# Optimization experiments

Measured on AMD Instinct MI355X. Metric: run time of the kernel, lower is better.

## Reference

```python
import jax, jax.numpy as jnp
import numpy as np

EPS_BN = 1e-5      # torch BatchNorm2d default eps
EPSILON = 1e-12    # signed-sqrt eps from the module
K = 3              # hardcoded k in forward


def _knn_idx(f, k):
    # f: [B, C, N] -> idx [B, N, k] of nearest neighbors (largest -dist^2)
    xx = jnp.sum(f * f, axis=1)                      # [B, N]
    inner = jnp.einsum('bcn,bcm->bnm', f, f)         # [B, N, N]
    pd = -xx[:, :, None] + 2.0 * inner - xx[:, None, :]
    return jax.lax.top_k(pd, k)[1]                   # [B, N, k]


def _graph_feature(f, k):
    # f: [B, C, N] -> [B, N, k, 2C] = concat(neighbor - center, center)
    idx = _knn_idx(f, k)
    ft = jnp.transpose(f, (0, 2, 1))                 # [B, N, C]
    neigh = jax.vmap(lambda x, i: x[i])(ft, idx)     # [B, N, k, C]
    center = jnp.broadcast_to(ft[:, :, None, :], neigh.shape)
    return jnp.concatenate([neigh - center, center], axis=-1)


def _edgeconv(f, W, gamma, beta, mean, var, k):
    # f: [B, C, N]; W: [O, 2C] (1x1 conv, no bias); eval-mode BN; LeakyReLU(0.2); max over k
    g = _graph_feature(f, k)                         # [B, N, k, 2C]
    y = jnp.einsum('bnkc,oc->bonk', g, W)            # [B, O, N, k]
    scale = (gamma / jnp.sqrt(var + EPS_BN))[None, :, None, None]
    y = (y - mean[None, :, None, None]) * scale + beta[None, :, None, None]
    y = jnp.where(y >= 0, y, 0.2 * y)                # LeakyReLU(0.2)
    return jnp.max(y, axis=-1)                       # [B, O, N]


def setup_inputs() -> dict:
    key = jax.random.key(0)
    ks = jax.random.split(key, 12)
    B, C, H, W, M = 64, 768, 26, 26, 32
    inp = {
        'features': jax.random.normal(ks[0], (B, C, H, W), jnp.float32),
        'attentions': jax.random.uniform(ks[1], (B, M, H, W), jnp.float32),
        'W1': jax.random.normal(ks[2], (C, 2 * C), jnp.float32) * 0.02,
        'gamma1': jax.random.uniform(ks[3], (C,), jnp.float32, 0.5, 1.5),
        'beta1': jax.random.normal(ks[4], (C,), jnp.float32) * 0.1,
        'mean1': jax.random.normal(ks[5], (C,), jnp.float32) * 0.1,
        'var1': jax.random.uniform(ks[6], (C,), jnp.float32, 0.5, 1.5),
        'W2': jax.random.normal(ks[7], (C, 2 * C), jnp.float32) * 0.02,
        'gamma2': jax.random.uniform(ks[8], (C,), jnp.float32, 0.5, 1.5),
        'beta2': jax.random.normal(ks[9], (C,), jnp.float32) * 0.1,
        'mean2': jax.random.normal(ks[10], (C,), jnp.float32) * 0.1,
        'var2': jax.random.uniform(ks[11], (C,), jnp.float32, 0.5, 1.5),
    }
    return inp


def reference(features, attentions, W1, gamma1, beta1, mean1, var1,
              W2, gamma2, beta2, mean2, var2):
    B = features.shape[0]
    # AdaptiveMaxPool2d(1) of features * attn_m, per attention map m.
    # lax.map over M avoids materializing the [B, M, C, H, W] product.
    def per_m(attn_m):                                # attn_m: [B, H, W]
        return jnp.max(features * attn_m[:, None, :, :], axis=(2, 3))  # [B, C]
    fm = jax.lax.map(per_m, jnp.transpose(attentions, (1, 0, 2, 3)))   # [M, B, C]
    fm = jnp.transpose(fm, (1, 2, 0))                 # [B, C, M]

    f1 = _edgeconv(fm, W1, gamma1, beta1, mean1, var1, K)   # [B, C, M]
    f2 = _edgeconv(f1, W2, gamma2, beta2, mean2, var2, K)   # [B, C, M]

    fuse = jnp.concatenate([f1, f2], axis=1).reshape(B, -1)  # [B, 2C*M]
    fuse = jnp.sign(fuse) * jnp.sqrt(jnp.abs(fuse) + EPSILON)
    norm = jnp.maximum(jnp.linalg.norm(fuse, axis=-1, keepdims=True), 1e-12)
    return fuse / norm
```

## Files before the change

kernel.cpp:

```cpp
#include <hip/hip_runtime.h>
#include <cfloat>
#include <cmath>

#define B_    64
#define C_    768
#define HW_   676
#define M_    32
#define TWOC_ 1536

__global__ __launch_bounds__(256) void pool_kernel(
    const float* __restrict__ feat, const float* __restrict__ attn,
    float* __restrict__ fm)
{
    const int b      = blockIdx.x / 12;
    const int cchunk = blockIdx.x % 12;
    const int t  = threadIdx.x;
    const int cl = t >> 2;
    const int m0 = (t & 3) * 8;
    const int c  = cchunk * 64 + cl;

    __shared__ float a_s[64][32];

    float acc[8];
#pragma unroll
    for (int j = 0; j < 8; ++j) acc[j] = -FLT_MAX;

    const float* fp = feat + ((size_t)b * C_ + c) * HW_;
    const float* ap = attn + (size_t)b * M_ * HW_;

    for (int hw0 = 0; hw0 < HW_; hw0 += 64) {
        const int hwlen = min(64, HW_ - hw0);
        __syncthreads();
        for (int idx = t; idx < 64 * 32; idx += 256) {
            int hw = idx >> 5, m = idx & 31;
            if (hw < hwlen) a_s[hw][m] = ap[m * HW_ + hw0 + hw];
        }
        __syncthreads();
        for (int hw = 0; hw < hwlen; hw += 4) {
            float4 f4 = *(const float4*)(fp + hw0 + hw);
            float fv[4] = {f4.x, f4.y, f4.z, f4.w};
#pragma unroll
            for (int q = 0; q < 4; ++q) {
                float f = fv[q];
#pragma unroll
                for (int j = 0; j < 8; ++j) {
                    float p = __fmul_rn(f, a_s[hw + q][m0 + j]);
                    acc[j] = fmaxf(acc[j], p);
                }
            }
        }
    }
    float* op = fm + ((size_t)b * C_ + c) * M_ + m0;
#pragma unroll
    for (int j = 0; j < 8; ++j) op[j] = acc[j];
}

__global__ __launch_bounds__(1024) void knn_kernel(
    const float* __restrict__ X, int* __restrict__ idxout)
{
    const int b = blockIdx.x;
    const int t = threadIdx.x;
    const int n = t >> 5, m = t & 31;

    __shared__ float xs[96][32];
    __shared__ float GF[32][32];
    __shared__ float G2[32][32];
    __shared__ float XS[32];
    __shared__ float XP[32];
    __shared__ float PA[32][32], PC[32][32], PDm[32][32];

    const float* Xb = X + (size_t)b * (C_ * M_);
    float accF = 0.f;
    float accP0 = 0.f, accP1 = 0.f;
    float accXs = 0.f;
    float leaf[8];

#pragma unroll
    for (int chunk = 0; chunk < 8; ++chunk) {
        __syncthreads();
        for (int i = t; i < 96 * 32; i += 1024)
            xs[i >> 5][i & 31] = Xb[(size_t)(chunk * 96 + (i >> 5)) * M_ + (i & 31)];
        __syncthreads();
#pragma unroll
        for (int c = 0; c < 96; ++c)
            accF = __fmaf_rn(xs[c][n], xs[c][m], accF);
        if (chunk < 4) {
#pragma unroll
            for (int c = 0; c < 96; ++c)
                accP0 = __fmaf_rn(xs[c][n], xs[c][m], accP0);
        } else {
#pragma unroll
            for (int c = 0; c < 96; ++c)
                accP1 = __fmaf_rn(xs[c][n], xs[c][m], accP1);
        }
        if (t < 32) {
#pragma unroll
            for (int c = 0; c < 96; ++c) {
                float v = xs[c][m];
                accXs = __fadd_rn(accXs, __fmul_rn(v, v));
            }
            float r[8];
#pragma unroll
            for (int j = 0; j < 8; ++j) {
                float v = xs[j][m];
                r[j] = __fmul_rn(v, v);
            }
            for (int i = 8; i < 96; i += 8) {
#pragma unroll
                for (int j = 0; j < 8; ++j) {
                    float v = xs[i + j][m];
                    r[j] = __fadd_rn(r[j], __fmul_rn(v, v));
                }
            }
            leaf[chunk] = __fadd_rn(
                __fadd_rn(__fadd_rn(r[0], r[1]), __fadd_rn(r[2], r[3])),
                __fadd_rn(__fadd_rn(r[4], r[5]), __fadd_rn(r[6], r[7])));
        }
    }
    GF[n][m] = accF;
    G2[n][m] = __fadd_rn(accP0, accP1);
    if (t < 32) {
        XS[m] = accXs;
        XP[m] = __fadd_rn(
            __fadd_rn(__fadd_rn(leaf[0], leaf[1]), __fadd_rn(leaf[2], leaf[3])),
            __fadd_rn(__fadd_rn(leaf[4], leaf[5]), __fadd_rn(leaf[6], leaf[7])));
    }
    __syncthreads();
    PA[n][m]  = __fsub_rn(__fadd_rn(-XS[n], 2.0f * GF[n][m]), XS[m]);
    PC[n][m]  = __fsub_rn(__fadd_rn(-XP[n], 2.0f * G2[n][m]), XP[m]);
    PDm[n][m] = __fsub_rn(__fadd_rn(-XP[n], 2.0f * GF[n][m]), XP[m]);
    __syncthreads();

    if (t < 32) {
        const int nn = t;
        const float* pa = PA[nn];
        const float* pc = PC[nn];
        const float* pd = PDm[nn];

        unsigned masks[3] = {0u, 0u, 0u};
        const float* rows[3] = {pa, pc, pd};
#pragma unroll
        for (int s = 0; s < 3; ++s) {
            unsigned chosen = 0;
            for (int p = 0; p < 3; ++p) {
                float best = -FLT_MAX; int bi = 0;
                for (int mm = 0; mm < 32; ++mm) {
                    if (chosen & (1u << mm)) continue;
                    float v = rows[s][mm];
                    if (v > best) { best = v; bi = mm; }
                }
                chosen |= 1u << bi;
            }
            masks[s] = chosen;
        }
        const unsigned mA = masks[0], mC = masks[1], mD = masks[2];

        unsigned chosen = 0;
        for (int p = 0; p < 3; ++p) {
            int bv = -1; float bp = -FLT_MAX; int bi = 0;
            for (int mm = 0; mm < 32; ++mm) {
                if (chosen & (1u << mm)) continue;
                int v = (int)((mA >> mm) & 1u) + (int)((mC >> mm) & 1u)
                      + (int)((mD >> mm) & 1u);
                float q = pd[mm];
                if (v > bv || (v == bv && q > bp)) { bv = v; bp = q; bi = mm; }
            }
            chosen |= 1u << bi;
            idxout[((size_t)b * 32 + nn) * 3 + p] = bi;
        }
    }
}

__global__ __launch_bounds__(256) void conv_kernel(
    const float* __restrict__ X, const float* __restrict__ W,
    const int* __restrict__ idx,
    const float* __restrict__ gamma, const float* __restrict__ beta,
    const float* __restrict__ mean,  const float* __restrict__ var,
    float* __restrict__ fout)
{
    const int b  = blockIdx.x / 12;
    const int oT = blockIdx.x % 12;
    const int o0 = oT * 64;
    const int t  = threadIdx.x;
    const int tx = t & 15;
    const int ty = t >> 4;

    __shared__ float fs_t[64][33];
    __shared__ float g_s[96][68];
    __shared__ float w_s[64][68];
    __shared__ int   idx_s[96];

    if (t < 96) idx_s[t] = idx[b * 96 + t];

    float acc[4][6] = {};

    const float* Xb = X + (size_t)b * (C_ * M_);

    for (int ct = 0; ct < 24; ++ct) {
        const int c0 = ct * 64;
        const bool diff = (c0 < C_);
        const int crow0 = diff ? c0 : (c0 - C_);
        __syncthreads();
        for (int e = t; e < 512; e += 256) {
            int cl = e >> 3, mq = (e & 7) * 4;
            float4 v = *(const float4*)(Xb + (size_t)(crow0 + cl) * M_ + mq);
            fs_t[cl][mq + 0] = v.x; fs_t[cl][mq + 1] = v.y;
            fs_t[cl][mq + 2] = v.z; fs_t[cl][mq + 3] = v.w;
        }
        for (int e = t; e < 1024; e += 256) {
            int o = e >> 4, cq = (e & 15) * 4;
            float4 v = *(const float4*)(W + (size_t)(o0 + o) * TWOC_ + c0 + cq);
            *(float4*)&w_s[o][cq] = v;
        }
        __syncthreads();
        for (int e = t; e < 96 * 64; e += 256) {
            int s = e >> 6, cl = e & 63;
            int n = s & 31, k = s >> 5;
            float v;
            if (diff) {
                int j = idx_s[n * 3 + k];
                v = __fsub_rn(fs_t[cl][j], fs_t[cl][n]);
            } else {
                v = fs_t[cl][n];
            }
            g_s[s][cl] = v;
        }
        __syncthreads();
        for (int c4 = 0; c4 < 64; c4 += 4) {
            float4 wv[4], gv[6];
#pragma unroll
            for (int i = 0; i < 4; ++i)
                wv[i] = *(const float4*)&w_s[ty * 4 + i][c4];
#pragma unroll
            for (int q = 0; q < 6; ++q)
                gv[q] = *(const float4*)&g_s[tx + 16 * q][c4];
#pragma unroll
            for (int i = 0; i < 4; ++i)
#pragma unroll
                for (int q = 0; q < 6; ++q) {
                    float a = acc[i][q];
                    a = __fmaf_rn(wv[i].x, gv[q].x, a);
                    a = __fmaf_rn(wv[i].y, gv[q].y, a);
                    a = __fmaf_rn(wv[i].z, gv[q].z, a);
                    a = __fmaf_rn(wv[i].w, gv[q].w, a);
                    acc[i][q] = a;
                }
        }
    }

#pragma unroll
    for (int i = 0; i < 4; ++i) {
        const int o = o0 + ty * 4 + i;
        const float sc = __fdiv_rn(gamma[o], __fsqrt_rn(__fadd_rn(var[o], 1e-5f)));
        const float mu = mean[o], be = beta[o];
#pragma unroll
        for (int half = 0; half < 2; ++half) {
            const int n = tx + 16 * half;
            float r = -FLT_MAX;
#pragma unroll
            for (int k = 0; k < 3; ++k) {
                float y = acc[i][2 * k + half];
                y = __fadd_rn(__fmul_rn(__fsub_rn(y, mu), sc), be);
                y = (y >= 0.f) ? y : __fmul_rn(0.2f, y);
                r = fmaxf(r, y);
            }
            fout[((size_t)b * C_ + o) * M_ + n] = r;
        }
    }
}

__global__ __launch_bounds__(256) void fuse_kernel(
    const float* __restrict__ f1, const float* __restrict__ f2,
    float* __restrict__ out)
{
    const int b = blockIdx.x;
    const int t = threadIdx.x;
    const float* p1 = f1 + (size_t)b * (C_ * M_);
    const float* p2 = f2 + (size_t)b * (C_ * M_);
    float* po = out + (size_t)b * (2 * C_ * M_);

    __shared__ double red[256];

    double lsum = 0.0;
    for (int i = t; i < 2 * C_ * M_; i += 256) {
        float x = (i < C_ * M_) ? p1[i] : p2[i - C_ * M_];
        float sq = __fsqrt_rn(__fadd_rn(fabsf(x), 1e-12f));
        float s = (x > 0.f) ? sq : ((x < 0.f) ? -sq : 0.f);
        lsum += (double)s * (double)s;
    }
    red[t] = lsum;
    __syncthreads();
    for (int off = 128; off > 0; off >>= 1) {
        if (t < off) red[t] += red[t + off];
        __syncthreads();
    }
    const float normf = fmaxf((float)sqrt(red[0]), 1e-12f);
    for (int i = t; i < 2 * C_ * M_; i += 256) {
        float x = (i < C_ * M_) ? p1[i] : p2[i - C_ * M_];
        float sq = __fsqrt_rn(__fadd_rn(fabsf(x), 1e-12f));
        float s = (x > 0.f) ? sq : ((x < 0.f) ? -sq : 0.f);
        po[i] = __fdiv_rn(s, normf);
    }
}

extern "C" void kernel_launch(void* const* d_in, const int* in_sizes, int n_in,
                              void* d_out, int out_size, void* d_ws, size_t ws_size,
                              hipStream_t stream)
{
    const float* feat = (const float*)d_in[0];
    const float* attn = (const float*)d_in[1];
    const float* W1   = (const float*)d_in[2];
    const float* g1   = (const float*)d_in[3];
    const float* be1  = (const float*)d_in[4];
    const float* mu1  = (const float*)d_in[5];
    const float* va1  = (const float*)d_in[6];
    const float* W2   = (const float*)d_in[7];
    const float* g2   = (const float*)d_in[8];
    const float* be2  = (const float*)d_in[9];
    const float* mu2  = (const float*)d_in[10];
    const float* va2  = (const float*)d_in[11];

    const size_t FM = (size_t)B_ * C_ * M_;
    float* fm  = (float*)d_ws;
    float* f1  = fm + FM;
    float* f2  = f1 + FM;
    int* idx1  = (int*)(f2 + FM);
    int* idx2  = idx1 + B_ * M_ * 3;

    pool_kernel<<<dim3(768), dim3(256), 0, stream>>>(feat, attn, fm);
    knn_kernel<<<dim3(64), dim3(1024), 0, stream>>>(fm, idx1);
    conv_kernel<<<dim3(768), dim3(256), 0, stream>>>(fm, W1, idx1, g1, be1, mu1, va1, f1);
    knn_kernel<<<dim3(64), dim3(1024), 0, stream>>>(f1, idx2);
    conv_kernel<<<dim3(768), dim3(256), 0, stream>>>(f1, W2, idx2, g2, be2, mu2, va2, f2);
    fuse_kernel<<<dim3(64), dim3(256), 0, stream>>>(f1, f2, (float*)d_out);
}
```

Measured before the change: 1.120 ms.

## Stage features in shared memory for pooling and widen conv output tile

The pooling kernel now loads both the feature and attention tiles into padded shared memory with coalesced float4 loads. Each thread covers 16 attention maps and reads float4 attention rows, where before each thread made strided per-channel global feature reads. The conv kernel doubles its output-channel tile to 128 per block with 8x6 accumulators per thread, so each block reuses the gathered graph features across twice as many outputs and the grid is halved. The trade-off is more registers and shared memory per block, fewer blocks in flight, and fewer threads in the pooling kernel.

```diff
diff --git a/kernel.cpp b/kernel.cpp
--- a/kernel.cpp
+++ b/kernel.cpp
@@ -8,51 +8,59 @@
 #define M_    32
 #define TWOC_ 1536
 
-__global__ __launch_bounds__(256) void pool_kernel(
+__global__ __launch_bounds__(128) void pool_kernel(
     const float* __restrict__ feat, const float* __restrict__ attn,
     float* __restrict__ fm)
 {
     const int b      = blockIdx.x / 12;
     const int cchunk = blockIdx.x % 12;
     const int t  = threadIdx.x;
-    const int cl = t >> 2;
-    const int m0 = (t & 3) * 8;
-    const int c  = cchunk * 64 + cl;
-
-    __shared__ float a_s[64][32];
-
-    float acc[8];
-#pragma unroll
-    for (int j = 0; j < 8; ++j) acc[j] = -FLT_MAX;
-
-    const float* fp = feat + ((size_t)b * C_ + c) * HW_;
+    const int cl = t >> 1;
+    const int mh = (t & 1) * 16;
+
+    __shared__ float a_s[32][68];
+    __shared__ float f_s[64][68];
+
+    float acc[16];
+#pragma unroll
+    for (int j = 0; j < 16; ++j) acc[j] = -FLT_MAX;
+
     const float* ap = attn + (size_t)b * M_ * HW_;
+    const float* fp = feat + ((size_t)b * C_ + cchunk * 64) * HW_;
 
     for (int hw0 = 0; hw0 < HW_; hw0 += 64) {
         const int hwlen = min(64, HW_ - hw0);
         __syncthreads();
-        for (int idx = t; idx < 64 * 32; idx += 256) {
-            int hw = idx >> 5, m = idx & 31;
-            if (hw < hwlen) a_s[hw][m] = ap[m * HW_ + hw0 + hw];
+        for (int e = t; e < 512; e += 128) {
+            int m = e >> 4, hq = (e & 15) * 4;
+            if (hq < hwlen)
+                *(float4*)&a_s[m][hq] =
+                    *(const float4*)(ap + (size_t)m * HW_ + hw0 + hq);
+        }
+        for (int e = t; e < 1024; e += 128) {
+            int r = e >> 4, hq = (e & 15) * 4;
+            if (hq < hwlen)
+                *(float4*)&f_s[r][hq] =
+                    *(const float4*)(fp + (size_t)r * HW_ + hw0 + hq);
         }
         __syncthreads();
         for (int hw = 0; hw < hwlen; hw += 4) {
-            float4 f4 = *(const float4*)(fp + hw0 + hw);
-            float fv[4] = {f4.x, f4.y, f4.z, f4.w};
-#pragma unroll
-            for (int q = 0; q < 4; ++q) {
-                float f = fv[q];
-#pragma unroll
-                for (int j = 0; j < 8; ++j) {
-                    float p = __fmul_rn(f, a_s[hw + q][m0 + j]);
-                    acc[j] = fmaxf(acc[j], p);
-                }
-            }
-        }
-    }
-    float* op = fm + ((size_t)b * C_ + c) * M_ + m0;
-#pragma unroll
-    for (int j = 0; j < 8; ++j) op[j] = acc[j];
+            float4 fv = *(const float4*)&f_s[cl][hw];
+#pragma unroll
+            for (int jm = 0; jm < 16; ++jm) {
+                float4 av = *(const float4*)&a_s[mh + jm][hw];
+                acc[jm] = fmaxf(acc[jm], __fmul_rn(fv.x, av.x));
+                acc[jm] = fmaxf(acc[jm], __fmul_rn(fv.y, av.y));
+                acc[jm] = fmaxf(acc[jm], __fmul_rn(fv.z, av.z));
+                acc[jm] = fmaxf(acc[jm], __fmul_rn(fv.w, av.w));
+            }
+        }
+    }
+    float* op = fm + ((size_t)b * C_ + cchunk * 64 + cl) * M_ + mh;
+#pragma unroll
+    for (int j = 0; j < 4; ++j)
+        *(float4*)(op + j * 4) = make_float4(acc[j*4+0], acc[j*4+1],
+                                             acc[j*4+2], acc[j*4+3]);
 }
 
 __global__ __launch_bounds__(1024) void knn_kernel(
@@ -178,21 +186,21 @@
     const float* __restrict__ mean,  const float* __restrict__ var,
     float* __restrict__ fout)
 {
-    const int b  = blockIdx.x / 12;
-    const int oT = blockIdx.x % 12;
-    const int o0 = oT * 64;
+    const int b  = blockIdx.x / 6;
+    const int oT = blockIdx.x % 6;
+    const int o0 = oT * 128;
     const int t  = threadIdx.x;
     const int tx = t & 15;
     const int ty = t >> 4;
 
     __shared__ float fs_t[64][33];
     __shared__ float g_s[96][68];
-    __shared__ float w_s[64][68];
+    __shared__ float w_s[128][68];
     __shared__ int   idx_s[96];
 
     if (t < 96) idx_s[t] = idx[b * 96 + t];
 
-    float acc[4][6] = {};
+    float acc[8][6] = {};
 
     const float* Xb = X + (size_t)b * (C_ * M_);
 
@@ -207,7 +215,7 @@
             fs_t[cl][mq + 0] = v.x; fs_t[cl][mq + 1] = v.y;
             fs_t[cl][mq + 2] = v.z; fs_t[cl][mq + 3] = v.w;
         }
-        for (int e = t; e < 1024; e += 256) {
+        for (int e = t; e < 2048; e += 256) {
             int o = e >> 4, cq = (e & 15) * 4;
             float4 v = *(const float4*)(W + (size_t)(o0 + o) * TWOC_ + c0 + cq);
             *(float4*)&w_s[o][cq] = v;
@@ -227,30 +235,29 @@
         }
         __syncthreads();
         for (int c4 = 0; c4 < 64; c4 += 4) {
-            float4 wv[4], gv[6];
-#pragma unroll
-            for (int i = 0; i < 4; ++i)
-                wv[i] = *(const float4*)&w_s[ty * 4 + i][c4];
+            float4 gv[6];
 #pragma unroll
             for (int q = 0; q < 6; ++q)
                 gv[q] = *(const float4*)&g_s[tx + 16 * q][c4];
 #pragma unroll
-            for (int i = 0; i < 4; ++i)
+            for (int i = 0; i < 8; ++i) {
+                float4 wv = *(const float4*)&w_s[i * 16 + ty][c4];
 #pragma unroll
                 for (int q = 0; q < 6; ++q) {
                     float a = acc[i][q];
-                    a = __fmaf_rn(wv[i].x, gv[q].x, a);
-                    a = __fmaf_rn(wv[i].y, gv[q].y, a);
-                    a = __fmaf_rn(wv[i].z, gv[q].z, a);
-                    a = __fmaf_rn(wv[i].w, gv[q].w, a);
+                    a = __fmaf_rn(wv.x, gv[q].x, a);
+                    a = __fmaf_rn(wv.y, gv[q].y, a);
+                    a = __fmaf_rn(wv.z, gv[q].z, a);
+                    a = __fmaf_rn(wv.w, gv[q].w, a);
                     acc[i][q] = a;
                 }
-        }
-    }
-
-#pragma unroll
-    for (int i = 0; i < 4; ++i) {
-        const int o = o0 + ty * 4 + i;
+            }
+        }
+    }
+
+#pragma unroll
+    for (int i = 0; i < 8; ++i) {
+        const int o = o0 + i * 16 + ty;
         const float sc = __fdiv_rn(gamma[o], __fsqrt_rn(__fadd_rn(var[o], 1e-5f)));
         const float mu = mean[o], be = beta[o];
 #pragma unroll
@@ -327,10 +334,10 @@
     int* idx1  = (int*)(f2 + FM);
     int* idx2  = idx1 + B_ * M_ * 3;
 
-    pool_kernel<<<dim3(768), dim3(256), 0, stream>>>(feat, attn, fm);
+    pool_kernel<<<dim3(768), dim3(128), 0, stream>>>(feat, attn, fm);
     knn_kernel<<<dim3(64), dim3(1024), 0, stream>>>(fm, idx1);
-    conv_kernel<<<dim3(768), dim3(256), 0, stream>>>(fm, W1, idx1, g1, be1, mu1, va1, f1);
+    conv_kernel<<<dim3(384), dim3(256), 0, stream>>>(fm, W1, idx1, g1, be1, mu1, va1, f1);
     knn_kernel<<<dim3(64), dim3(1024), 0, stream>>>(f1, idx2);
-    conv_kernel<<<dim3(768), dim3(256), 0, stream>>>(f1, W2, idx2, g2, be2, mu2, va2, f2);
+    conv_kernel<<<dim3(384), dim3(256), 0, stream>>>(f1, W2, idx2, g2, be2, mu2, va2, f2);
     fuse_kernel<<<dim3(64), dim3(256), 0, stream>>>(f1, f2, (float*)d_out);
 }
```

New measurement: 1.160 ms. +3.5%, slower.
